# Optimization experiments

Measured on AMD Instinct MI355X. Metric: run time of the kernel, lower is better.

## Reference

```python
import jax, jax.numpy as jnp
import numpy as np

N_CLASSES = 3
FEAT_SIZES = (64, 32)  # source1 64x64, source2 32x32 for 512x512 input


def conv(x, w, b):
    # x: NCHW, w: OIHW, 3x3 SAME, stride 1
    y = jax.lax.conv_general_dilated(
        x, w, window_strides=(1, 1), padding='SAME',
        dimension_numbers=('NCHW', 'OIHW', 'NCHW'))
    return y + b[None, :, None, None]


def maxpool(x):
    return jax.lax.reduce_window(x, -jnp.inf, jax.lax.max,
                                 (1, 1, 2, 2), (1, 1, 2, 2), 'VALID')


def l2norm(x, gamma, eps=1e-10):
    # standard SSD L2Norm: per-position channel L2 normalize, learned per-channel scale
    n = jnp.sqrt(jnp.sum(x * x, axis=1, keepdims=True)) + eps
    return gamma[None, :, None, None] * x / n


def make_priors():
    # PriorBox: one prior per feature-map cell, normalized (cx, cy) centers
    ps = []
    for f in FEAT_SIZES:
        c = (jnp.arange(f, dtype=jnp.float32) + 0.5) / f
        cy, cx = jnp.meshgrid(c, c, indexing='ij')
        ps.append(jnp.stack([cx.ravel(), cy.ravel()], axis=1))  # [f*f, 2]
    return jnp.concatenate(ps, axis=0)  # [5120, 2]


def setup_inputs() -> dict:
    key = jax.random.key(0)
    ks = iter(jax.random.split(key, 32))

    def he(k, shape):
        fan_in = shape[1] * shape[2] * shape[3]
        return jax.random.normal(k, shape, jnp.float32) * (2.0 / fan_in) ** 0.5

    d = {'x': jax.random.normal(next(ks), (8, 2, 512, 512), jnp.float32)}
    shapes = [(64, 2, 3, 3), (64, 64, 3, 3), (128, 64, 3, 3), (128, 128, 3, 3),
              (256, 128, 3, 3), (256, 256, 3, 3), (256, 256, 3, 3), (256, 256, 3, 3)]
    for n, s in enumerate(shapes, 1):
        d[f'w{n}'] = he(next(ks), s)
        d[f'b{n}'] = jnp.zeros((s[0],), jnp.float32)
    d['g1'] = 20.0 * jnp.ones((256,), jnp.float32)  # L2Norm1 weight
    d['g2'] = 20.0 * jnp.ones((256,), jnp.float32)  # L2Norm2 weight
    for pre, oc in (('l', 2), ('c', N_CLASSES), ('r', 1)):
        for si in (1, 2):
            d[f'{pre}w{si}'] = he(next(ks), (oc, 256, 3, 3))
            d[f'{pre}b{si}'] = jnp.zeros((oc,), jnp.float32)
    return d


def reference(x, w1, b1, w2, b2, w3, b3, w4, b4, w5, b5, w6, b6, w7, b7, w8, b8,
              g1, g2, lw1, lb1, lw2, lb2, cw1, cb1, cw2, cb2, rw1, rb1, rw2, rb2):
    B = x.shape[0]
    r = jax.nn.relu
    # vgg[0:33]
    x = r(conv(x, w1, b1)); x = r(conv(x, w2, b2)); x = maxpool(x)
    x = r(conv(x, w3, b3)); x = r(conv(x, w4, b4)); x = maxpool(x)
    x = r(conv(x, w5, b5)); x = r(conv(x, w6, b6)); x = maxpool(x)
    s1 = l2norm(x, g1)                 # [B,256,64,64]
    # vgg[33:]
    x = maxpool(x)
    x = r(conv(x, w7, b7)); x = r(conv(x, w8, b8))
    s2 = l2norm(x, g2)                 # [B,256,32,32]

    def head(s, w_, b_):
        # conv -> permute(0,2,3,1) -> flatten, as in the torch forward
        return conv(s, w_, b_).transpose(0, 2, 3, 1).reshape(B, -1)

    loc = jnp.concatenate([head(s1, lw1, lb1), head(s2, lw2, lb2)], 1).reshape(B, -1, 2)
    conf = jnp.concatenate([head(s1, cw1, cb1), head(s2, cw2, cb2)], 1).reshape(B, -1, N_CLASSES)
    regr = jnp.concatenate([head(s1, rw1, rb1), head(s2, rw2, rb2)], 1).reshape(B, -1, 1)
    priors = make_priors()
    return loc, conf, regr, priors
```

## Files before the change

kernel.cpp:

```cpp
#include <hip/hip_runtime.h>

typedef _Float16 f16;
typedef _Float16 f16x8 __attribute__((ext_vector_type(8)));
typedef float f32x4 __attribute__((ext_vector_type(4)));

__device__ __forceinline__ f32x4 mfma16(f16x8 a, f16x8 b, f32x4 c) {
    return __builtin_amdgcn_mfma_f32_16x16x32_f16(a, b, c, 0, 0, 0);
}

template<int N>
__device__ __forceinline__ void waitcnt_vm() {
    asm volatile("s_waitcnt vmcnt(%0)" :: "i"(N) : "memory");
}

template<int IC, int OC, int BX, int WY, int WO, int MT, int NT, bool POOL>
__global__ __launch_bounds__(WY * WO * 64) void convmf_k(
    const f16* __restrict__ in, const f16* __restrict__ wt,
    const float* __restrict__ bias, f16* __restrict__ out,
    int H, int W, int ocBlocks, long inStride, long outStride)
{
    constexpr int WAVES = WY * WO;
    constexpr int HALVES = WAVES / 4;
    constexpr int WROWS = MT * 16 / BX;
    constexpr int BROWS = WROWS * WY;
    constexpr int SR = BROWS + 2;
    constexpr int SC = BX + 2;
    constexpr int LOG = (BX == 64) ? 6 : 5;
    constexpr int NPIX = SR * SC;
    constexpr int STRD = 64 * HALVES;
    constexpr int NISS = (NPIX + STRD - 1) / STRD;
    constexpr int NPpad = NISS * STRD;
    constexpr int NC = IC / 32;
    static_assert(WAVES == 4 || WAVES == 8, "4 or 8 waves");
    static_assert(!POOL || (BX == 64 && MT == 8), "pool path assumes BX==64, MT==8");
    __shared__ f16 lds[2 * 4 * NPpad * 8];

    const int tid  = threadIdx.x;
    const int lane = tid & 63;
    const int wv   = tid >> 6;
    const int wy   = wv / WO;
    const int wo   = wv % WO;
    const int part = wv & 3;
    const int half = wv >> 2;
    const int lm   = lane & 15;
    const int lk   = lane >> 4;
    const int x0   = blockIdx.x * BX;
    const int y0   = blockIdx.y * BROWS;
    const int zb   = blockIdx.z;
    const int n    = zb / ocBlocks;
    const int oc0  = (zb - n * ocBlocks) * (16 * NT * WO) + wo * (16 * NT);
    in  += (long)n * inStride;
    out += (long)n * outStride;

    const int Wp = W + 2;
    const f16* ipBase = in + ((long)y0 * Wp + x0) * IC + part * 8;

    auto STAGE = [&](int ch, int bi) {
        const f16* ip = ipBase + ch * 32;
#pragma unroll
        for (int i = 0; i < NISS; ++i) {
            int p = i * STRD + half * 64 + lane;
            int pc = (p < NPIX) ? p : 0;
            int r = pc / SC, xcol = pc - r * SC;
            __builtin_amdgcn_global_load_lds(
                (const __attribute__((address_space(1))) void*)(ip + ((long)r * Wp + xcol) * IC),
                (__attribute__((address_space(3))) void*)&lds[((bi * 4 + part) * NPpad + i * STRD + half * 64) * 8],
                16, 0, 0);
        }
    };

    f32x4 acc[MT][NT];
#pragma unroll
    for (int mt = 0; mt < MT; ++mt)
#pragma unroll
        for (int nt = 0; nt < NT; ++nt)
            acc[mt][nt] = (f32x4){0.f, 0.f, 0.f, 0.f};

    STAGE(0, 0);
#pragma unroll
    for (int c = 0; c < NC; ++c) {
        const int cur = c & 1;
        if (c + 1 < NC) {
            STAGE(c + 1, cur ^ 1);
            waitcnt_vm<NISS>();
        } else {
            waitcnt_vm<0>();
        }
        __syncthreads();

        const int ic0 = c * 32;
        for (int t = 0; t < 9; ++t) {
            int dy = t / 3, dx = t - dy * 3;
            const f16* wp = wt + ((long)t * OC + oc0) * IC + ic0 + lk * 8;
            f16x8 bfr[NT];
#pragma unroll
            for (int nt = 0; nt < NT; ++nt)
                bfr[nt] = *(const f16x8*)(wp + (nt * 16 + lm) * IC);
#pragma unroll
            for (int mt = 0; mt < MT; ++mt) {
                int pos = mt * 16 + lm;
                int xx = pos & (BX - 1);
                int yy = wy * WROWS + (pos >> LOG);
                int pp = (yy + dy) * SC + xx + dx;
                f16x8 a = *(const f16x8*)&lds[((cur * 4 + lk) * NPpad + pp) * 8];
#pragma unroll
                for (int nt = 0; nt < NT; ++nt)
                    acc[mt][nt] = mfma16(a, bfr[nt], acc[mt][nt]);
            }
        }
        __syncthreads();
    }

    if constexpr (!POOL) {
#pragma unroll
        for (int nt = 0; nt < NT; ++nt) {
            int oc = oc0 + nt * 16 + lm;
            float bs = bias[oc];
#pragma unroll
            for (int mt = 0; mt < MT; ++mt) {
#pragma unroll
                for (int r = 0; r < 4; ++r) {
                    int pos = mt * 16 + lk * 4 + r;
                    int xx = pos & (BX - 1);
                    int yy = wy * WROWS + (pos >> LOG);
                    float v = fmaxf(acc[mt][nt][r] + bs, 0.f);
                    out[((long)(y0 + yy + 1) * (W + 2) + (x0 + xx + 1)) * OC + oc] = (f16)v;
                }
            }
        }
    } else {
        const int Wo = W >> 1;
#pragma unroll
        for (int nt = 0; nt < NT; ++nt) {
            int oc = oc0 + nt * 16 + lm;
            float bs = bias[oc];
#pragma unroll
            for (int mt = 0; mt < 4; ++mt) {
#pragma unroll
                for (int r = 0; r < 4; r += 2) {
                    float v = fmaxf(fmaxf(acc[mt][nt][r], acc[mt][nt][r + 1]),
                                    fmaxf(acc[mt + 4][nt][r], acc[mt + 4][nt][r + 1]));
                    v = fmaxf(v + bs, 0.f);
                    int pos = mt * 16 + lk * 4 + r;
                    int xo = pos >> 1;
                    out[((long)((y0 >> 1) + wy + 1) * (Wo + 2) + ((x0 >> 1) + xo + 1)) * OC + oc] = (f16)v;
                }
            }
        }
    }
}

__global__ __launch_bounds__(256) void convmf1_k(
    const float* __restrict__ x, int itemBase,
    const f16* __restrict__ wt1,
    const float* __restrict__ bias, f16* __restrict__ out, long outStride)
{
    __shared__ f16 ldsx[10 * 66 * 2];
    __shared__ f16 ldsa[512 * 40];
    const int tid = threadIdx.x;
    const int lane = tid & 63;
    const int wv = tid >> 6;
    const int lm = lane & 15;
    const int lk = lane >> 4;
    const int x0 = blockIdx.x * 64;
    const int y0 = blockIdx.y * 8;
    const float* xb = x + (long)(itemBase + blockIdx.z) * 2 * 512 * 512;
    out += (long)blockIdx.z * outStride;

    for (int s = tid; s < 660; s += 256) {
        int r = s / 66, xc = s - r * 66;
        int gy = y0 + r - 1, gx = x0 + xc - 1;
        f16 v0 = (f16)0.f, v1 = (f16)0.f;
        if ((unsigned)gy < 512u && (unsigned)gx < 512u) {
            v0 = (f16)xb[(long)gy * 512 + gx];
            v1 = (f16)xb[262144 + (long)gy * 512 + gx];
        }
        ldsx[(r * 66 + xc) * 2]     = v0;
        ldsx[(r * 66 + xc) * 2 + 1] = v1;
    }
    __syncthreads();
    for (int s = tid; s < 2048; s += 256) {
        int pos = s >> 2, g = s & 3;
        int row = pos >> 6, col = pos & 63;
        f16x8 v;
#pragma unroll
        for (int j = 0; j < 8; ++j) {
            int k = g * 8 + j;
            f16 val = (f16)0.f;
            if (k < 18) {
                int t = k >> 1, ic = k & 1;
                int dy = t / 3, dx = t - dy * 3;
                val = ldsx[((row + dy) * 66 + col + dx) * 2 + ic];
            }
            v[j] = val;
        }
        *(f16x8*)&ldsa[pos * 40 + g * 8] = v;
    }
    __syncthreads();

    f32x4 acc[8][4];
#pragma unroll
    for (int mt = 0; mt < 8; ++mt)
#pragma unroll
        for (int nt = 0; nt < 4; ++nt)
            acc[mt][nt] = (f32x4){0.f, 0.f, 0.f, 0.f};

    f16x8 b0 = *(const f16x8*)(wt1 + (0 * 16 + lm) * 32 + lk * 8);
    f16x8 b1 = *(const f16x8*)(wt1 + (1 * 16 + lm) * 32 + lk * 8);
    f16x8 b2 = *(const f16x8*)(wt1 + (2 * 16 + lm) * 32 + lk * 8);
    f16x8 b3 = *(const f16x8*)(wt1 + (3 * 16 + lm) * 32 + lk * 8);
#pragma unroll
    for (int mt = 0; mt < 8; ++mt) {
        int pos = wv * 128 + mt * 16 + lm;
        f16x8 a = *(const f16x8*)&ldsa[pos * 40 + lk * 8];
        acc[mt][0] = mfma16(a, b0, acc[mt][0]);
        acc[mt][1] = mfma16(a, b1, acc[mt][1]);
        acc[mt][2] = mfma16(a, b2, acc[mt][2]);
        acc[mt][3] = mfma16(a, b3, acc[mt][3]);
    }
#pragma unroll
    for (int nt = 0; nt < 4; ++nt) {
        int oc = nt * 16 + lm;
        float bs = bias[oc];
#pragma unroll
        for (int mt = 0; mt < 8; ++mt) {
#pragma unroll
            for (int r = 0; r < 4; ++r) {
                int pos = wv * 128 + mt * 16 + lk * 4 + r;
                int xx = pos & 63, yy = pos >> 6;
                float v = fmaxf(acc[mt][nt][r] + bs, 0.f);
                out[((long)(y0 + yy + 1) * 514 + (x0 + xx + 1)) * 64 + oc] = (f16)v;
            }
        }
    }
}

template<int BX>
__global__ __launch_bounds__(256) void headconv_k(
    const f16* __restrict__ s, long sStride, const f16* __restrict__ wth,
    const float* __restrict__ lb, const float* __restrict__ cb, const float* __restrict__ rb,
    float* __restrict__ loc, float* __restrict__ conf, float* __restrict__ regr,
    int W, int posoff)
{
    constexpr int BY = (BX == 64) ? 1 : 2;
    constexpr int SR = BY + 2, SC = BX + 2;
    constexpr int LOG = (BX == 64) ? 6 : 5;
    __shared__ f16 lds[SR * SC * 40];
    const int tid = threadIdx.x;
    const int lane = tid & 63;
    const int wv = tid >> 6;
    const int lm = lane & 15;
    const int lk = lane >> 4;
    const int y0 = blockIdx.y * BY;
    const int b = blockIdx.z;
    s += (long)b * sStride;

    f32x4 acc = (f32x4){0.f, 0.f, 0.f, 0.f};
    const int Wp = W + 2;
    for (int ic0 = 0; ic0 < 256; ic0 += 32) {
        if (ic0) __syncthreads();
        const f16* ip = s + (long)y0 * Wp * 256 + ic0;
        constexpr int TASKS = SR * SC * 4;
        for (int t = tid; t < TASKS; t += 256) {
            int r = t / (SC * 4);
            int rem = t - r * (SC * 4);
            int xcol = rem >> 2, g = rem & 3;
            f16x8 v = *(const f16x8*)(ip + ((long)r * Wp + xcol) * 256 + g * 8);
            *(f16x8*)&lds[(r * SC + xcol) * 40 + g * 8] = v;
        }
        __syncthreads();
        for (int t = 0; t < 9; ++t) {
            int dy = t / 3, dx = t - dy * 3;
            f16x8 bf = *(const f16x8*)(wth + ((long)t * 16 + lm) * 256 + ic0 + lk * 8);
            int pos = wv * 16 + lm;
            int xx = pos & (BX - 1), yy = pos >> LOG;
            f16x8 a = *(const f16x8*)&lds[((yy + dy) * SC + xx + dx) * 40 + lk * 8];
            acc = mfma16(a, bf, acc);
        }
    }
#pragma unroll
    for (int r = 0; r < 4; ++r) {
        int pos = wv * 16 + lk * 4 + r;
        int xx = pos & (BX - 1), yy = pos >> LOG;
        int P = posoff + (y0 + yy) * W + xx;
        float v = acc[r];
        if (lm < 2)       loc[((long)b * 5120 + P) * 2 + lm]       = v + lb[lm];
        else if (lm < 5)  conf[((long)b * 5120 + P) * 3 + (lm - 2)] = v + cb[lm - 2];
        else if (lm == 5) regr[(long)b * 5120 + P]                  = v + rb[0];
    }
}

__global__ __launch_bounds__(256) void cvt_wt_k(const float* __restrict__ w, f16* __restrict__ wt,
                                                int OC, int IC)
{
    int idx = blockIdx.x * 256 + threadIdx.x;
    if (idx >= OC * IC) return;
    int oc = idx / IC, ic = idx - oc * IC;
#pragma unroll
    for (int t = 0; t < 9; ++t)
        wt[((long)t * OC + oc) * IC + ic] = (f16)w[(long)idx * 9 + t];
}

__global__ __launch_bounds__(64) void cvt_wt1_k(const float* __restrict__ w, f16* __restrict__ wt1)
{
    int oc = threadIdx.x;
#pragma unroll
    for (int k = 0; k < 32; ++k) {
        f16 v = (f16)0.f;
        if (k < 18) {
            int t = k >> 1, ic = k & 1;
            v = (f16)w[((long)oc * 2 + ic) * 9 + t];
        }
        wt1[oc * 32 + k] = v;
    }
}

__global__ __launch_bounds__(256) void cvt_wth_k(const float* __restrict__ lw, const float* __restrict__ cw,
                                                 const float* __restrict__ rw, f16* __restrict__ wth)
{
    int idx = blockIdx.x * 256 + threadIdx.x;
    if (idx >= 9 * 16 * 256) return;
    int t = idx / (16 * 256);
    int r = (idx / 256) & 15;
    int ic = idx & 255;
    float v = 0.f;
    if (r < 2)      v = lw[((long)r * 256 + ic) * 9 + t];
    else if (r < 5) v = cw[((long)(r - 2) * 256 + ic) * 9 + t];
    else if (r == 5) v = rw[(long)ic * 9 + t];
    wth[((long)t * 16 + r) * 256 + ic] = (f16)v;
}

__global__ __launch_bounds__(256) void halo_k(f16* __restrict__ buf, int W, int H, int C,
                                              long stride, int items)
{
    int per = (2 * (W + 2) + 2 * H) * C;
    long total = (long)per * items;
    long idx = (long)blockIdx.x * 256 + threadIdx.x;
    if (idx >= total) return;
    int n = idx / per;
    int j = idx - (long)n * per;
    int c = j % C, p = j / C;
    int row, col;
    if (p < W + 2) { row = 0; col = p; }
    else if (p < 2 * (W + 2)) { row = H + 1; col = p - (W + 2); }
    else { int q = p - 2 * (W + 2); row = 1 + (q >> 1); col = (q & 1) ? (W + 1) : 0; }
    buf[(long)n * stride + ((long)row * (W + 2) + col) * C + c] = (f16)0.f;
}

__global__ __launch_bounds__(256) void l2n_k(const f16* __restrict__ in, const float* __restrict__ g,
                                             f16* __restrict__ out, int W, long stride, int total)
{
    int i = blockIdx.x * 256 + threadIdx.x;
    if (i >= total) return;
    int b = i / (W * W);
    int rem = i - b * W * W;
    int y = rem / W, x = rem - y * W;
    long off = (long)b * stride + ((long)(y + 1) * (W + 2) + x + 1) * 256;
    const f16* p = in + off;
    f16* q = out + off;
    float s = 0.f;
    for (int gg = 0; gg < 32; ++gg) {
        f16x8 v = *(const f16x8*)(p + gg * 8);
#pragma unroll
        for (int j = 0; j < 8; ++j) { float f = (float)v[j]; s = fmaf(f, f, s); }
    }
    float inv = 1.f / (sqrtf(s) + 1e-10f);
    for (int gg = 0; gg < 32; ++gg) {
        f16x8 v = *(const f16x8*)(p + gg * 8);
        f16x8 o;
#pragma unroll
        for (int j = 0; j < 8; ++j) o[j] = (f16)(g[gg * 8 + j] * ((float)v[j] * inv));
        *(f16x8*)(q + gg * 8) = o;
    }
}

__global__ __launch_bounds__(256) void mp_k(const f16* __restrict__ in, f16* __restrict__ out)
{
    int idx = blockIdx.x * 256 + threadIdx.x;
    if (idx >= 8 * 32 * 32 * 32) return;
    int gg = idx & 31;
    int xo = (idx >> 5) & 31;
    int yo = (idx >> 10) & 31;
    int b = idx >> 15;
    const f16* p = in + (long)b * 1115136 + ((long)(2 * yo + 1) * 66 + 2 * xo + 1) * 256 + gg * 8;
    f16x8 a0 = *(const f16x8*)p;
    f16x8 a1 = *(const f16x8*)(p + 256);
    f16x8 a2 = *(const f16x8*)(p + 66 * 256);
    f16x8 a3 = *(const f16x8*)(p + 66 * 256 + 256);
    f16x8 o;
#pragma unroll
    for (int j = 0; j < 8; ++j)
        o[j] = (f16)fmaxf(fmaxf((float)a0[j], (float)a1[j]), fmaxf((float)a2[j], (float)a3[j]));
    *(f16x8*)(out + (long)b * 295936 + ((long)(yo + 1) * 34 + xo + 1) * 256 + gg * 8) = o;
}

__global__ __launch_bounds__(256) void priors_k(float* __restrict__ out)
{
    int r = blockIdx.x * 256 + threadIdx.x;
    if (r >= 5120) return;
    float cx, cy;
    if (r < 4096) {
        int i = r >> 6, j = r & 63;
        cx = (j + 0.5f) / 64.0f; cy = (i + 0.5f) / 64.0f;
    } else {
        int rr = r - 4096;
        int i = rr >> 5, j = rr & 31;
        cx = (j + 0.5f) / 32.0f; cy = (i + 0.5f) / 32.0f;
    }
    out[2 * r] = cx;
    out[2 * r + 1] = cy;
}

extern "C" void kernel_launch(void* const* d_in, const int* in_sizes, int n_in,
                              void* d_out, int out_size, void* d_ws, size_t ws_size,
                              hipStream_t stream)
{
    const float* x  = (const float*)d_in[0];
    const float* w1 = (const float*)d_in[1];  const float* b1 = (const float*)d_in[2];
    const float* w2 = (const float*)d_in[3];  const float* b2 = (const float*)d_in[4];
    const float* w3 = (const float*)d_in[5];  const float* b3 = (const float*)d_in[6];
    const float* w4 = (const float*)d_in[7];  const float* b4 = (const float*)d_in[8];
    const float* w5 = (const float*)d_in[9];  const float* b5 = (const float*)d_in[10];
    const float* w6 = (const float*)d_in[11]; const float* b6 = (const float*)d_in[12];
    const float* w7 = (const float*)d_in[13]; const float* b7 = (const float*)d_in[14];
    const float* w8 = (const float*)d_in[15]; const float* b8 = (const float*)d_in[16];
    const float* g1 = (const float*)d_in[17]; const float* g2 = (const float*)d_in[18];
    const float* lw1 = (const float*)d_in[19]; const float* lb1 = (const float*)d_in[20];
    const float* lw2 = (const float*)d_in[21]; const float* lb2 = (const float*)d_in[22];
    const float* cw1 = (const float*)d_in[23]; const float* cb1 = (const float*)d_in[24];
    const float* cw2 = (const float*)d_in[25]; const float* cb2 = (const float*)d_in[26];
    const float* rw1 = (const float*)d_in[27]; const float* rb1 = (const float*)d_in[28];
    const float* rw2 = (const float*)d_in[29]; const float* rb2 = (const float*)d_in[30];

    f16* wsh = (f16*)d_ws;
    f16* wt2  = wsh + 0;
    f16* wt3  = wsh + 36864;
    f16* wt4  = wsh + 110592;
    f16* wt5  = wsh + 258048;
    f16* wt6  = wsh + 552960;
    f16* wt7  = wsh + 1142784;
    f16* wt8  = wsh + 1732608;
    f16* wt1  = wsh + 2322432;
    f16* wth1 = wsh + 2324480;
    f16* wth2 = wsh + 2361344;
    f16* x6p  = wsh + 2398208;
    const long PI = 11319296;

    const long A1S = 16908544;
    const long P1S = 4260096;
    const long A3S = 8520192;
    const long P2S = 2163200;
    const long A5S = 4326400;
    const long PH2 = 18391040;

    int G = 1;
    for (int g = 8; g >= 1; g >>= 1) {
        long ext = (long)g * (A1S + P1S); if (ext < PH2) ext = PH2;
        if (2.0 * (double)(PI + ext) <= (double)ws_size) { G = g; break; }
    }
    const int NGRP = 8 / G;

    f16* a1 = wsh + PI;
    f16* p1 = wsh + PI + (long)G * A1S;
    f16* a3 = a1;
    f16* p2 = p1;
    f16* a5 = a1;
    f16* s1 = wsh + PI;
    f16* p4 = wsh + PI + 8921088;
    f16* a7 = wsh + PI + 11288576;
    f16* a8 = wsh + PI + 13656064;
    f16* s2 = wsh + PI + 16023552;

    float* loc  = (float*)d_out;
    float* conf = loc + 81920;
    float* regr = loc + 204800;
    float* pri  = loc + 245760;

    cvt_wt_k<<<dim3((64 * 64 + 255) / 256), 256, 0, stream>>>(w2, wt2, 64, 64);
    cvt_wt_k<<<dim3((128 * 64 + 255) / 256), 256, 0, stream>>>(w3, wt3, 128, 64);
    cvt_wt_k<<<dim3((128 * 128 + 255) / 256), 256, 0, stream>>>(w4, wt4, 128, 128);
    cvt_wt_k<<<dim3((256 * 128 + 255) / 256), 256, 0, stream>>>(w5, wt5, 256, 128);
    cvt_wt_k<<<dim3((256 * 256 + 255) / 256), 256, 0, stream>>>(w6, wt6, 256, 256);
    cvt_wt_k<<<dim3((256 * 256 + 255) / 256), 256, 0, stream>>>(w7, wt7, 256, 256);
    cvt_wt_k<<<dim3((256 * 256 + 255) / 256), 256, 0, stream>>>(w8, wt8, 256, 256);
    cvt_wt1_k<<<dim3(1), 64, 0, stream>>>(w1, wt1);
    cvt_wth_k<<<dim3(144), 256, 0, stream>>>(lw1, cw1, rw1, wth1);
    cvt_wth_k<<<dim3(144), 256, 0, stream>>>(lw2, cw2, rw2, wth2);

    for (int grp = 0; grp < NGRP; ++grp) {
        f16* x6g = x6p + (long)grp * G * 1115136;
        halo_k<<<dim3((G * (2 * 514 + 2 * 512) * 64 + 255) / 256), 256, 0, stream>>>(a1, 512, 512, 64, A1S, G);
        halo_k<<<dim3((G * (2 * 258 + 2 * 256) * 64 + 255) / 256), 256, 0, stream>>>(p1, 256, 256, 64, P1S, G);
        convmf1_k<<<dim3(8, 64, G), 256, 0, stream>>>(x, grp * G, wt1, b1, a1, A1S);
        convmf_k<64, 64, 64, 2, 4, 8, 1, true><<<dim3(8, 128, G), 512, 0, stream>>>(
            a1, wt2, b2, p1, 512, 512, 1, A1S, P1S);
        halo_k<<<dim3((G * (2 * 258 + 2 * 256) * 128 + 255) / 256), 256, 0, stream>>>(a3, 256, 256, 128, A3S, G);
        convmf_k<64, 128, 64, 2, 4, 8, 2, false><<<dim3(4, 64, G), 512, 0, stream>>>(
            p1, wt3, b3, a3, 256, 256, 1, P1S, A3S);
        halo_k<<<dim3((G * (2 * 130 + 2 * 128) * 128 + 255) / 256), 256, 0, stream>>>(p2, 128, 128, 128, P2S, G);
        convmf_k<128, 128, 64, 2, 4, 8, 2, true><<<dim3(4, 64, G), 512, 0, stream>>>(
            a3, wt4, b4, p2, 256, 256, 1, A3S, P2S);
        halo_k<<<dim3((G * (2 * 130 + 2 * 128) * 256 + 255) / 256), 256, 0, stream>>>(a5, 128, 128, 256, A5S, G);
        convmf_k<128, 256, 64, 2, 4, 8, 1, false><<<dim3(2, 32, 4 * G), 512, 0, stream>>>(
            p2, wt5, b5, a5, 128, 128, 4, P2S, A5S);
        convmf_k<256, 256, 64, 2, 4, 8, 1, true><<<dim3(2, 32, 4 * G), 512, 0, stream>>>(
            a5, wt6, b6, x6g, 128, 128, 4, A5S, 1115136);
    }

    halo_k<<<dim3((8 * (2 * 66 + 2 * 64) * 256 + 255) / 256), 256, 0, stream>>>(s1, 64, 64, 256, 1115136, 8);
    halo_k<<<dim3((8 * (2 * 34 + 2 * 32) * 256 + 255) / 256), 256, 0, stream>>>(p4, 32, 32, 256, 295936, 8);
    halo_k<<<dim3((8 * (2 * 34 + 2 * 32) * 256 + 255) / 256), 256, 0, stream>>>(a7, 32, 32, 256, 295936, 8);
    halo_k<<<dim3((8 * (2 * 34 + 2 * 32) * 256 + 255) / 256), 256, 0, stream>>>(s2, 32, 32, 256, 295936, 8);

    l2n_k<<<dim3((32768 + 255) / 256), 256, 0, stream>>>(x6p, g1, s1, 64, 1115136, 32768);
    mp_k<<<dim3((262144 + 255) / 256), 256, 0, stream>>>(x6p, p4);
    convmf_k<256, 256, 32, 2, 2, 4, 4, false><<<dim3(1, 8, 16), 256, 0, stream>>>(
        p4, wt7, b7, a7, 32, 32, 2, 295936, 295936);
    convmf_k<256, 256, 32, 2, 2, 4, 4, false><<<dim3(1, 8, 16), 256, 0, stream>>>(
        a7, wt8, b8, a8, 32, 32, 2, 295936, 295936);
    l2n_k<<<dim3((8192 + 255) / 256), 256, 0, stream>>>(a8, g2, s2, 32, 295936, 8192);

    headconv_k<64><<<dim3(1, 64, 8), 256, 0, stream>>>(
        s1, 1115136, wth1, lb1, cb1, rb1, loc, conf, regr, 64, 0);
    headconv_k<32><<<dim3(1, 16, 8), 256, 0, stream>>>(
        s2, 295936, wth2, lb2, cb2, rb2, loc, conf, regr, 32, 4096);
    priors_k<<<dim3(20), 256, 0, stream>>>(pri);

    (void)in_sizes; (void)n_in; (void)out_size; (void)ws_size;
}
```

Before: 1.187 ms.

## Switch VGG conv kernels to 32x32x16 MFMA with 32-wide pixel tiles

Replaces the 16x16x32 MFMA conv kernel with one using the 32x32x16 f16 MFMA. Each wave now computes two 32-pixel rows by NT 32-channel output tiles, so spatial tiles are 32 columns wide. All layer launch grids and block shapes change to match. The intent is higher MFMA throughput and fewer LDS and weight fragment loads per FLOP. The risks are higher accumulator register pressure, more halo overhead from narrower tiles, and a changed epilogue and pool indexing that must match the 32x32 output layout.

```diff
diff --git a/kernel.cpp b/kernel.cpp
--- a/kernel.cpp
+++ b/kernel.cpp
@@ -3,9 +3,13 @@
 typedef _Float16 f16;
 typedef _Float16 f16x8 __attribute__((ext_vector_type(8)));
 typedef float f32x4 __attribute__((ext_vector_type(4)));
+typedef float f32x16 __attribute__((ext_vector_type(16)));
 
 __device__ __forceinline__ f32x4 mfma16(f16x8 a, f16x8 b, f32x4 c) {
     return __builtin_amdgcn_mfma_f32_16x16x32_f16(a, b, c, 0, 0, 0);
+}
+__device__ __forceinline__ f32x16 mfma32(f16x8 a, f16x8 b, f32x16 c) {
+    return __builtin_amdgcn_mfma_f32_32x32x16_f16(a, b, c, 0, 0, 0);
 }
 
 template<int N>
@@ -13,26 +17,23 @@
     asm volatile("s_waitcnt vmcnt(%0)" :: "i"(N) : "memory");
 }
 
-template<int IC, int OC, int BX, int WY, int WO, int MT, int NT, bool POOL>
-__global__ __launch_bounds__(WY * WO * 64) void convmf_k(
+template<int IC, int OC, int WY, int WO, int NT, bool POOL>
+__global__ __launch_bounds__(WY * WO * 64) void convmf32_k(
     const f16* __restrict__ in, const f16* __restrict__ wt,
     const float* __restrict__ bias, f16* __restrict__ out,
     int H, int W, int ocBlocks, long inStride, long outStride)
 {
     constexpr int WAVES = WY * WO;
-    constexpr int HALVES = WAVES / 4;
-    constexpr int WROWS = MT * 16 / BX;
-    constexpr int BROWS = WROWS * WY;
+    constexpr int HALVES = (WAVES + 3) / 4;
+    constexpr int BROWS = 2 * WY;
     constexpr int SR = BROWS + 2;
-    constexpr int SC = BX + 2;
-    constexpr int LOG = (BX == 64) ? 6 : 5;
+    constexpr int SC = 34;
     constexpr int NPIX = SR * SC;
     constexpr int STRD = 64 * HALVES;
     constexpr int NISS = (NPIX + STRD - 1) / STRD;
     constexpr int NPpad = NISS * STRD;
     constexpr int NC = IC / 32;
     static_assert(WAVES == 4 || WAVES == 8, "4 or 8 waves");
-    static_assert(!POOL || (BX == 64 && MT == 8), "pool path assumes BX==64, MT==8");
     __shared__ f16 lds[2 * 4 * NPpad * 8];
 
     const int tid  = threadIdx.x;
@@ -42,13 +43,13 @@
     const int wo   = wv % WO;
     const int part = wv & 3;
     const int half = wv >> 2;
-    const int lm   = lane & 15;
-    const int lk   = lane >> 4;
-    const int x0   = blockIdx.x * BX;
+    const int m    = lane & 31;
+    const int hi   = lane >> 5;
+    const int x0   = blockIdx.x * 32;
     const int y0   = blockIdx.y * BROWS;
     const int zb   = blockIdx.z;
     const int n    = zb / ocBlocks;
-    const int oc0  = (zb - n * ocBlocks) * (16 * NT * WO) + wo * (16 * NT);
+    const int oc0  = (zb - n * ocBlocks) * (32 * NT * WO) + wo * (32 * NT);
     in  += (long)n * inStride;
     out += (long)n * outStride;
 
@@ -69,12 +70,13 @@
         }
     };
 
-    f32x4 acc[MT][NT];
-#pragma unroll
-    for (int mt = 0; mt < MT; ++mt)
+    f32x16 acc[2][NT];
+#pragma unroll
+    for (int mt = 0; mt < 2; ++mt)
 #pragma unroll
         for (int nt = 0; nt < NT; ++nt)
-            acc[mt][nt] = (f32x4){0.f, 0.f, 0.f, 0.f};
+#pragma unroll
+            for (int r = 0; r < 16; ++r) acc[mt][nt][r] = 0.f;
 
     STAGE(0, 0);
 #pragma unroll
@@ -91,21 +93,24 @@
         const int ic0 = c * 32;
         for (int t = 0; t < 9; ++t) {
             int dy = t / 3, dx = t - dy * 3;
-            const f16* wp = wt + ((long)t * OC + oc0) * IC + ic0 + lk * 8;
-            f16x8 bfr[NT];
-#pragma unroll
-            for (int nt = 0; nt < NT; ++nt)
-                bfr[nt] = *(const f16x8*)(wp + (nt * 16 + lm) * IC);
-#pragma unroll
-            for (int mt = 0; mt < MT; ++mt) {
-                int pos = mt * 16 + lm;
-                int xx = pos & (BX - 1);
-                int yy = wy * WROWS + (pos >> LOG);
-                int pp = (yy + dy) * SC + xx + dx;
-                f16x8 a = *(const f16x8*)&lds[((cur * 4 + lk) * NPpad + pp) * 8];
+#pragma unroll
+            for (int kh = 0; kh < 2; ++kh) {
+                f16x8 bfr[NT];
 #pragma unroll
                 for (int nt = 0; nt < NT; ++nt)
-                    acc[mt][nt] = mfma16(a, bfr[nt], acc[mt][nt]);
+                    bfr[nt] = *(const f16x8*)(wt + ((long)t * OC + oc0 + nt * 32 + m) * IC
+                                              + ic0 + kh * 16 + hi * 8);
+                f16x8 afr[2];
+#pragma unroll
+                for (int mt = 0; mt < 2; ++mt) {
+                    int pp = (wy * 2 + mt + dy) * SC + (m + dx);
+                    afr[mt] = *(const f16x8*)&lds[((cur * 4 + kh * 2 + hi) * NPpad + pp) * 8];
+                }
+#pragma unroll
+                for (int mt = 0; mt < 2; ++mt)
+#pragma unroll
+                    for (int nt = 0; nt < NT; ++nt)
+                        acc[mt][nt] = mfma32(afr[mt], bfr[nt], acc[mt][nt]);
             }
         }
         __syncthreads();
@@ -114,37 +119,34 @@
     if constexpr (!POOL) {
 #pragma unroll
         for (int nt = 0; nt < NT; ++nt) {
-            int oc = oc0 + nt * 16 + lm;
+            int oc = oc0 + nt * 32 + m;
             float bs = bias[oc];
 #pragma unroll
-            for (int mt = 0; mt < MT; ++mt) {
-#pragma unroll
-                for (int r = 0; r < 4; ++r) {
-                    int pos = mt * 16 + lk * 4 + r;
-                    int xx = pos & (BX - 1);
-                    int yy = wy * WROWS + (pos >> LOG);
-                    float v = fmaxf(acc[mt][nt][r] + bs, 0.f);
-                    out[((long)(y0 + yy + 1) * (W + 2) + (x0 + xx + 1)) * OC + oc] = (f16)v;
+            for (int mt = 0; mt < 2; ++mt) {
+                int y = y0 + wy * 2 + mt;
+#pragma unroll
+                for (int reg = 0; reg < 16; ++reg) {
+                    int row = (reg & 3) + 8 * (reg >> 2) + 4 * hi;
+                    float v = fmaxf(acc[mt][nt][reg] + bs, 0.f);
+                    out[((long)(y + 1) * (W + 2) + (x0 + row + 1)) * OC + oc] = (f16)v;
                 }
             }
         }
     } else {
         const int Wo = W >> 1;
+        const int orow = (y0 >> 1) + wy;
 #pragma unroll
         for (int nt = 0; nt < NT; ++nt) {
-            int oc = oc0 + nt * 16 + lm;
+            int oc = oc0 + nt * 32 + m;
             float bs = bias[oc];
 #pragma unroll
-            for (int mt = 0; mt < 4; ++mt) {
-#pragma unroll
-                for (int r = 0; r < 4; r += 2) {
-                    float v = fmaxf(fmaxf(acc[mt][nt][r], acc[mt][nt][r + 1]),
-                                    fmaxf(acc[mt + 4][nt][r], acc[mt + 4][nt][r + 1]));
-                    v = fmaxf(v + bs, 0.f);
-                    int pos = mt * 16 + lk * 4 + r;
-                    int xo = pos >> 1;
-                    out[((long)((y0 >> 1) + wy + 1) * (Wo + 2) + ((x0 >> 1) + xo + 1)) * OC + oc] = (f16)v;
-                }
+            for (int reg = 0; reg < 16; reg += 2) {
+                float v = fmaxf(fmaxf(acc[0][nt][reg], acc[0][nt][reg + 1]),
+                                fmaxf(acc[1][nt][reg], acc[1][nt][reg + 1]));
+                v = fmaxf(v + bs, 0.f);
+                int row = (reg & 3) + 8 * (reg >> 2) + 4 * hi;
+                int ocol = (x0 >> 1) + (row >> 1);
+                out[((long)(orow + 1) * (Wo + 2) + (ocol + 1)) * OC + oc] = (f16)v;
             }
         }
     }
@@ -492,19 +494,19 @@
         halo_k<<<dim3((G * (2 * 514 + 2 * 512) * 64 + 255) / 256), 256, 0, stream>>>(a1, 512, 512, 64, A1S, G);
         halo_k<<<dim3((G * (2 * 258 + 2 * 256) * 64 + 255) / 256), 256, 0, stream>>>(p1, 256, 256, 64, P1S, G);
         convmf1_k<<<dim3(8, 64, G), 256, 0, stream>>>(x, grp * G, wt1, b1, a1, A1S);
-        convmf_k<64, 64, 64, 2, 4, 8, 1, true><<<dim3(8, 128, G), 512, 0, stream>>>(
+        convmf32_k<64, 64, 4, 1, 2, true><<<dim3(16, 64, G), 256, 0, stream>>>(
             a1, wt2, b2, p1, 512, 512, 1, A1S, P1S);
         halo_k<<<dim3((G * (2 * 258 + 2 * 256) * 128 + 255) / 256), 256, 0, stream>>>(a3, 256, 256, 128, A3S, G);
-        convmf_k<64, 128, 64, 2, 4, 8, 2, false><<<dim3(4, 64, G), 512, 0, stream>>>(
+        convmf32_k<64, 128, 2, 2, 2, false><<<dim3(8, 64, G), 256, 0, stream>>>(
             p1, wt3, b3, a3, 256, 256, 1, P1S, A3S);
         halo_k<<<dim3((G * (2 * 130 + 2 * 128) * 128 + 255) / 256), 256, 0, stream>>>(p2, 128, 128, 128, P2S, G);
-        convmf_k<128, 128, 64, 2, 4, 8, 2, true><<<dim3(4, 64, G), 512, 0, stream>>>(
+        convmf32_k<128, 128, 2, 2, 2, true><<<dim3(8, 64, G), 256, 0, stream>>>(
             a3, wt4, b4, p2, 256, 256, 1, A3S, P2S);
         halo_k<<<dim3((G * (2 * 130 + 2 * 128) * 256 + 255) / 256), 256, 0, stream>>>(a5, 128, 128, 256, A5S, G);
-        convmf_k<128, 256, 64, 2, 4, 8, 1, false><<<dim3(2, 32, 4 * G), 512, 0, stream>>>(
-            p2, wt5, b5, a5, 128, 128, 4, P2S, A5S);
-        convmf_k<256, 256, 64, 2, 4, 8, 1, true><<<dim3(2, 32, 4 * G), 512, 0, stream>>>(
-            a5, wt6, b6, x6g, 128, 128, 4, A5S, 1115136);
+        convmf32_k<128, 256, 2, 4, 2, false><<<dim3(4, 32, G), 512, 0, stream>>>(
+            p2, wt5, b5, a5, 128, 128, 1, P2S, A5S);
+        convmf32_k<256, 256, 2, 4, 2, true><<<dim3(4, 32, G), 512, 0, stream>>>(
+            a5, wt6, b6, x6g, 128, 128, 1, A5S, 1115136);
     }
 
     halo_k<<<dim3((8 * (2 * 66 + 2 * 64) * 256 + 255) / 256), 256, 0, stream>>>(s1, 64, 64, 256, 1115136, 8);
@@ -514,9 +516,9 @@
 
     l2n_k<<<dim3((32768 + 255) / 256), 256, 0, stream>>>(x6p, g1, s1, 64, 1115136, 32768);
     mp_k<<<dim3((262144 + 255) / 256), 256, 0, stream>>>(x6p, p4);
-    convmf_k<256, 256, 32, 2, 2, 4, 4, false><<<dim3(1, 8, 16), 256, 0, stream>>>(
+    convmf32_k<256, 256, 2, 2, 2, false><<<dim3(1, 8, 16), 256, 0, stream>>>(
         p4, wt7, b7, a7, 32, 32, 2, 295936, 295936);
-    convmf_k<256, 256, 32, 2, 2, 4, 4, false><<<dim3(1, 8, 16), 256, 0, stream>>>(
+    convmf32_k<256, 256, 2, 2, 2, false><<<dim3(1, 8, 16), 256, 0, stream>>>(
         a7, wt8, b8, a8, 32, 32, 2, 295936, 295936);
     l2n_k<<<dim3((8192 + 255) / 256), 256, 0, stream>>>(a8, g2, s2, 32, 295936, 8192);
 
```

Measured after the change: 1.549 ms. 30.6% more time.
